# Performance work log

Measured on AMD Instinct MI355X. Metric: run time of the kernel, lower is better.

## Reference

```python
import jax, jax.numpy as jnp
import numpy as np
from jax import lax

NMS_RADIUS = 4
THRESHOLD = 0.005
BORDER = 4
MAX_KP = 1024


def _max_pool(x, r):
    # torch max_pool2d pads with -inf; reduce_window 'SAME' pads with init value.
    w = 2 * r + 1
    return lax.reduce_window(x, -jnp.inf, lax.max, (1, w, w), (1, 1, 1), 'SAME')


def simple_nms(scores, radius):
    zeros = jnp.zeros_like(scores)
    max_mask = scores == _max_pool(scores, radius)
    for _ in range(2):
        supp_mask = _max_pool(max_mask.astype(scores.dtype), radius) > 0
        supp_scores = jnp.where(supp_mask, zeros, scores)
        new_max_mask = supp_scores == _max_pool(supp_scores, radius)
        max_mask = max_mask | (new_max_mask & ~supp_mask)
    return jnp.where(max_mask, scores, zeros)


def sample_descriptors(kp, desc, s):
    """Bilinear grid_sample (align_corners=True, zero padding) + L2 normalize.
    kp: [B,N,2] (x,y) full-resolution pixel coords; desc: [B,C,h,w]."""
    b, c, h, w = desc.shape
    k = kp - s / 2 + 0.5
    gx = k[..., 0] / (w * s - 1) * 2.0 - 1.0
    gy = k[..., 1] / (h * s - 1) * 2.0 - 1.0
    x = (gx + 1.0) * 0.5 * (w - 1)  # align_corners=True mapping
    y = (gy + 1.0) * 0.5 * (h - 1)
    x0 = jnp.floor(x); y0 = jnp.floor(y)
    wx1 = x - x0; wy1 = y - y0
    x0i = x0.astype(jnp.int32); y0i = y0.astype(jnp.int32)

    def tap(d_b, xi, yi):  # d_b [C,h,w]; xi,yi [N] -> [C,N], zero outside
        v = ((xi >= 0) & (xi < w) & (yi >= 0) & (yi < h)).astype(d_b.dtype)
        g = d_b[:, jnp.clip(yi, 0, h - 1), jnp.clip(xi, 0, w - 1)]
        return g * v

    def one(d_b, x0i, y0i, wx1, wy1):
        wx0 = 1.0 - wx1; wy0 = 1.0 - wy1
        return (tap(d_b, x0i, y0i) * (wx0 * wy0)
                + tap(d_b, x0i + 1, y0i) * (wx1 * wy0)
                + tap(d_b, x0i, y0i + 1) * (wx0 * wy1)
                + tap(d_b, x0i + 1, y0i + 1) * (wx1 * wy1))

    out = jax.vmap(one)(desc, x0i, y0i, wx1, wy1)  # [B,C,N]
    n = jnp.maximum(jnp.linalg.norm(out, axis=1, keepdims=True), 1e-12)
    return out / n


def conv1x1(w, b, x):  # Conv1d kernel_size=1: [O,I] @ [B,I,N]
    return jnp.einsum('oi,bin->bon', w, x) + b[None, :, None]


def setup_inputs() -> dict:
    key = jax.random.key(0)
    ks = jax.random.split(key, 13)
    B, H, W = 4, 480, 640
    inp = {
        'scores': jax.random.uniform(ks[0], (B, H, W), jnp.float32),
        'd1': jax.random.normal(ks[1], (B, 64, H // 2, W // 2), jnp.float32),
        'd2': jax.random.normal(ks[2], (B, 128, H // 4, W // 4), jnp.float32),
        'cDa': jax.random.normal(ks[3], (B, 256, H // 8, W // 8), jnp.float32),
        'd4': jax.random.normal(ks[4], (B, 256, H // 16, W // 16), jnp.float32),
        'lin0_w': jax.random.normal(ks[5], (256, 256), jnp.float32) / np.sqrt(256),
        'lin0_b': jax.random.normal(ks[6], (256,), jnp.float32) * 0.01,
        'lin1_w': jax.random.normal(ks[7], (128, 128), jnp.float32) / np.sqrt(128),
        'lin1_b': jax.random.normal(ks[8], (128,), jnp.float32) * 0.01,
        'lin2_w': jax.random.normal(ks[9], (64, 64), jnp.float32) / np.sqrt(64),
        'lin2_b': jax.random.normal(ks[10], (64,), jnp.float32) * 0.01,
        'merge_w': jax.random.normal(ks[11], (256, 704), jnp.float32) / np.sqrt(704),
        'merge_b': jax.random.normal(ks[12], (256,), jnp.float32) * 0.01,
    }
    return inp


def reference(scores, d1, d2, cDa, d4, lin0_w, lin0_b, lin1_w, lin1_b,
              lin2_w, lin2_b, merge_w, merge_b):
    B, H, W = scores.shape
    s = simple_nms(scores, NMS_RADIUS)
    ys, xs = jnp.meshgrid(jnp.arange(H), jnp.arange(W), indexing='ij')
    valid = (ys >= BORDER) & (ys < H - BORDER) & (xs >= BORDER) & (xs < W - BORDER)
    masked = jnp.where(valid[None] & (s > THRESHOLD), s, -1.0)
    top_scores, idx = lax.top_k(masked.reshape(B, -1), MAX_KP)
    kx = (idx % W).astype(jnp.float32)
    ky = (idx // W).astype(jnp.float32)
    kp = jnp.stack([kx, ky], axis=-1)  # [B,K,2] (x,y), i.e. torch.flip(k,[1])
    de1 = sample_descriptors(kp, d1, 2)    # [B,64,K]
    de2 = sample_descriptors(kp, d2, 4)    # [B,128,K]
    de3 = sample_descriptors(kp, cDa, 8)   # [B,256,K]
    de4 = sample_descriptors(kp, d4, 16)   # [B,256,K]
    de4 = conv1x1(lin0_w, lin0_b, de4)
    de2 = conv1x1(lin1_w, lin1_b, de2)
    de1 = conv1x1(lin2_w, lin2_b, de1)
    descriptors = conv1x1(merge_w, merge_b,
                          jnp.concatenate([de1, de2, de3, de4], axis=1))
    return kp, top_scores, descriptors
```

## Files before the change

kernel.cpp:

```cpp
#include <hip/hip_runtime.h>
#include <hip/hip_bf16.h>

#define B 4
#define H 480
#define W 640
#define HW (H*W)
#define BHW (B*H*W)
#define NKP 1024
#define THRESH 0.005f
#define CAP 16384
#define NCOL (B*NKP)
#define KTOT 704

typedef __attribute__((ext_vector_type(8))) short s8v;
typedef __attribute__((ext_vector_type(4))) float f4v;
typedef struct { float x, y; } __attribute__((aligned(4))) f2u;

__device__ __forceinline__ short f2bf(float f) {
    __hip_bfloat16 h = __float2bfloat16(f);
    return *(short*)&h;
}

__device__ __forceinline__ float max3f(float a, float b, float c) {
    return fmaxf(fmaxf(a, b), c);
}
#define MAX9(A, base, str) \
    max3f(max3f((A)[(base)], (A)[(base)+(str)], (A)[(base)+2*(str)]), \
          max3f((A)[(base)+3*(str)], (A)[(base)+4*(str)], (A)[(base)+5*(str)]), \
          max3f((A)[(base)+6*(str)], (A)[(base)+7*(str)], (A)[(base)+8*(str)]))

__global__ void fuse_all(const float* __restrict__ merge_w, const float* __restrict__ merge_b,
                         const float* __restrict__ lin0_w, const float* __restrict__ lin0_b,
                         const float* __restrict__ lin1_w, const float* __restrict__ lin1_b,
                         const float* __restrict__ lin2_w, const float* __restrict__ lin2_b,
                         short* __restrict__ Mw, float* __restrict__ biasf, int* __restrict__ cnt) {
    if (blockIdx.x == 704) {
        int o = threadIdx.x;
        if (o < 4) cnt[o * 64] = 0;
        float acc = merge_b[o];
        for (int k = 0; k < 64; ++k)  acc += merge_w[o * KTOT + k] * lin2_b[k];
        for (int k = 0; k < 128; ++k) acc += merge_w[o * KTOT + 64 + k] * lin1_b[k];
        for (int k = 0; k < 256; ++k) acc += merge_w[o * KTOT + 448 + k] * lin0_b[k];
        biasf[o] = acc;
        return;
    }
    int e = blockIdx.x * 256 + threadIdx.x;
    int o = e / KTOT;
    int j = e - o * KTOT;
    float acc = 0.0f;
    if (j < 64) {
        for (int k = 0; k < 64; ++k) acc += merge_w[o * KTOT + k] * lin2_w[k * 64 + j];
    } else if (j < 192) {
        int jj = j - 64;
        for (int k = 0; k < 128; ++k) acc += merge_w[o * KTOT + 64 + k] * lin1_w[k * 128 + jj];
    } else if (j < 448) {
        acc = merge_w[o * KTOT + j];
    } else {
        int jj = j - 448;
        for (int k = 0; k < 256; ++k) acc += merge_w[o * KTOT + 448 + k] * lin0_w[k * 256 + jj];
    }
    Mw[o * KTOT + j] = f2bf(acc);
}

__global__ __launch_bounds__(256) void nms1(const float* __restrict__ scores,
                                            float* __restrict__ mask) {
    __shared__ float tile[40][40];
    __shared__ float hm[40][32];
    int bz = blockIdx.z;
    int x0 = blockIdx.x * 32, y0 = blockIdx.y * 32;
    const float* sp = scores + bz * HW;
    for (int t = threadIdx.x; t < 1600; t += 256) {
        int ly = t / 40, lx = t - ly * 40;
        int gy = y0 - 4 + ly, gx = x0 - 4 + lx;
        tile[ly][lx] = (gy >= 0 && gy < H && gx >= 0 && gx < W) ? sp[gy * W + gx] : -INFINITY;
    }
    __syncthreads();
    for (int t = threadIdx.x; t < 1280; t += 256) {
        int ly = t >> 5, lx = t & 31;
        hm[ly][lx] = MAX9(&tile[ly][0], lx, 1);
    }
    __syncthreads();
    for (int t = threadIdx.x; t < 1024; t += 256) {
        int ly = t >> 5, lx = t & 31;
        float m = MAX9(&hm[0][0], ly * 32 + lx, 32);
        float s = tile[ly + 4][lx + 4];
        mask[bz * HW + (y0 + ly) * W + x0 + lx] = (s == m) ? 1.0f : 0.0f;
    }
}

__global__ __launch_bounds__(512) void nms2_compact(const float* __restrict__ scores,
                                                    const float* __restrict__ mask0,
                                                    unsigned long long* __restrict__ cand,
                                                    int* __restrict__ cnt) {
    __shared__ float Sm[56 * 56];
    __shared__ float Mm[64 * 64];
    __shared__ float Zm[56 * 56];
    __shared__ float Tm[64 * 56];
    __shared__ int lcnt, gbase;
    int bz = blockIdx.z;
    int x0 = blockIdx.x * 32, y0 = blockIdx.y * 32;
    const float* sp = scores + bz * HW;
    const float* mp = mask0 + bz * HW;
    if (threadIdx.x == 0) lcnt = 0;
    for (int t = threadIdx.x; t < 4096; t += 512) {
        int ly = t >> 6, lx = t & 63;
        int gy = y0 - 16 + ly, gx = x0 - 16 + lx;
        Mm[t] = (gy >= 0 && gy < H && gx >= 0 && gx < W) ? mp[gy * W + gx] : 0.0f;
    }
    for (int t = threadIdx.x; t < 3136; t += 512) {
        int i = t / 56, j = t - i * 56;
        int gy = y0 - 12 + i, gx = x0 - 12 + j;
        Sm[t] = (gy >= 0 && gy < H && gx >= 0 && gx < W) ? sp[gy * W + gx] : -1.0f;
    }
    __syncthreads();
    for (int t = threadIdx.x; t < 3584; t += 512) {
        int i = t / 56, c = t - i * 56;
        Tm[i * 56 + c] = MAX9(Mm, i * 64 + c, 1);
    }
    __syncthreads();
    for (int t = threadIdx.x; t < 3136; t += 512) {
        int i = t / 56, c = t - i * 56;
        float m = MAX9(Tm, i * 56 + c, 56);
        Zm[t] = (m > 0.0f) ? -1.0f : Sm[t];
    }
    __syncthreads();
    for (int t = threadIdx.x; t < 2688; t += 512) {
        int i = t / 48, c = t - i * 48;
        Tm[i * 56 + c] = MAX9(Zm, i * 56 + c, 1);
    }
    __syncthreads();
    for (int t = threadIdx.x; t < 2304; t += 512) {
        int r = t / 48, c = t - r * 48;
        float m = MAX9(Tm, r * 56 + c, 56);
        float Zc = Zm[(r + 4) * 56 + c + 4];
        int mi = (r + 8) * 64 + c + 8;
        bool nm = (Zc == m) && (Zc >= 0.0f);
        Mm[mi] = (Mm[mi] != 0.0f || nm) ? 1.0f : 0.0f;
    }
    __syncthreads();
    for (int t = threadIdx.x; t < 1920; t += 512) {
        int r = t / 40, c = t - r * 40;
        Tm[r * 56 + c] = MAX9(Mm, (r + 8) * 64 + c + 8, 1);
    }
    __syncthreads();
    for (int t = threadIdx.x; t < 1600; t += 512) {
        int r = t / 40, c = t - r * 40;
        float m = MAX9(Tm, r * 56 + c, 56);
        int zi = (r + 8) * 56 + c + 8;
        Zm[zi] = (m > 0.0f) ? -1.0f : Sm[zi];
    }
    __syncthreads();
    for (int t = threadIdx.x; t < 1280; t += 512) {
        int r = t / 32, c = t & 31;
        Tm[r * 56 + c] = MAX9(Zm, (r + 8) * 56 + c + 8, 1);
    }
    __syncthreads();
    unsigned long long keys[2];
    int nl = 0;
    #pragma unroll
    for (int q = 0; q < 2; ++q) {
        int t = threadIdx.x + q * 512;
        int r3 = t >> 5, c = t & 31;
        float m = MAX9(Tm, r3 * 56 + c, 56);
        float Zc = Zm[(r3 + 12) * 56 + c + 12];
        bool fin = (Mm[(r3 + 16) * 64 + c + 16] != 0.0f) || ((Zc == m) && (Zc >= 0.0f));
        int gy = y0 + r3, gx = x0 + c;
        float sc = Sm[(r3 + 12) * 56 + c + 12];
        if (fin && gy >= 4 && gy < H - 4 && gx >= 4 && gx < W - 4 && sc > THRESH) {
            unsigned r = (unsigned)(gy * W + gx);
            unsigned bits = __float_as_uint(sc) | 0x80000000u;
            keys[nl++] = ((unsigned long long)bits << 32) |
                         (unsigned long long)(0xFFFFFFFFu - r);
        }
    }
    int lpos = 0;
    if (nl) lpos = atomicAdd(&lcnt, nl);
    __syncthreads();
    if (threadIdx.x == 0) gbase = (lcnt > 0) ? atomicAdd(&cnt[bz * 64], lcnt) : 0;
    __syncthreads();
    for (int j = 0; j < nl; ++j) {
        int p = gbase + lpos + j;
        if (p < CAP) cand[(size_t)bz * CAP + p] = keys[j];
    }
}

__global__ __launch_bounds__(1024) void topk(const unsigned long long* __restrict__ cand,
                                             const int* __restrict__ cnt,
                                             float* __restrict__ out, int* __restrict__ fidx,
                                             int* __restrict__ perm) {
    __shared__ int hist[2048];
    __shared__ unsigned long long buf[4096];
    __shared__ int scnt, spiv1, spiv2, sabove;
    int b = blockIdx.x, tid = threadIdx.x;
    int m = cnt[b * 64]; if (m > CAP) m = CAP;
    const unsigned long long* cb = cand + (size_t)b * CAP;
    int target = (m < 1024) ? m : 1024;

    hist[tid] = 0; hist[tid + 1024] = 0;
    if (tid == 0) { scnt = 0; spiv1 = 2048; spiv2 = 0; sabove = 0; }
    __syncthreads();
    for (int i = tid; i < m; i += 1024)
        atomicAdd(&hist[(int)(cb[i] >> 53) & 0x7FF], 1);
    __syncthreads();
    for (int d = 1; d < 2048; d <<= 1) {
        int v0 = hist[tid] + ((tid + d < 2048) ? hist[tid + d] : 0);
        int v1 = hist[tid + 1024] + ((tid + 1024 + d < 2048) ? hist[tid + 1024 + d] : 0);
        __syncthreads();
        hist[tid] = v0; hist[tid + 1024] = v1;
        __syncthreads();
    }
    if (target > 0) {
        for (int t = tid; t < 2048; t += 1024) {
            int c = hist[t];
            int cn = (t < 2047) ? hist[t + 1] : 0;
            if (c >= target && cn < target) { spiv1 = t; sabove = cn; }
        }
    }
    __syncthreads();
    int piv1 = spiv1;
    int target2 = target - sabove;
    hist[tid] = 0; hist[tid + 1024] = 0;
    __syncthreads();
    for (int i = tid; i < m; i += 1024) {
        unsigned long long k = cb[i];
        if (((int)(k >> 53) & 0x7FF) == piv1)
            atomicAdd(&hist[(int)(k >> 42) & 0x7FF], 1);
    }
    __syncthreads();
    for (int d = 1; d < 2048; d <<= 1) {
        int v0 = hist[tid] + ((tid + d < 2048) ? hist[tid + d] : 0);
        int v1 = hist[tid + 1024] + ((tid + 1024 + d < 2048) ? hist[tid + 1024 + d] : 0);
        __syncthreads();
        hist[tid] = v0; hist[tid + 1024] = v1;
        __syncthreads();
    }
    if (target > 0) {
        for (int t = tid; t < 2048; t += 1024) {
            int c = hist[t];
            int cn = (t < 2047) ? hist[t + 1] : 0;
            if (c >= target2 && cn < target2) spiv2 = t;
        }
    }
    __syncthreads();
    int piv2 = spiv2;
    for (int i = tid; i < m; i += 1024) {
        unsigned long long k = cb[i];
        int b1 = (int)(k >> 53) & 0x7FF;
        bool sel = (target > 0) &&
                   (b1 > piv1 || (b1 == piv1 && (((int)(k >> 42) & 0x7FF) >= piv2)));
        if (sel) {
            int p = atomicAdd(&scnt, 1);
            if (p < 4096) buf[p] = k;
        }
    }
    __syncthreads();
    int sc_ = scnt; if (sc_ > 4096) sc_ = 4096;
    int ns = 1024; while (ns < sc_) ns <<= 1;
    for (int t = tid; t < ns; t += 1024) if (t >= sc_) buf[t] = 0ULL;
    __syncthreads();
    for (int k = 2; k <= ns; k <<= 1)
        for (int j = k >> 1; j > 0; j >>= 1) {
            __syncthreads();
            for (int t = tid; t < ns; t += 1024) {
                int ixj = t ^ j;
                if (ixj > t) {
                    unsigned long long a = buf[t], bb = buf[ixj];
                    if (((t & k) == 0) ? (a < bb) : (a > bb)) { buf[t] = bb; buf[ixj] = a; }
                }
            }
        }
    __syncthreads();
    unsigned long long key = buf[tid];
    float kx, ky, sc;
    unsigned idx;
    if (key != 0ULL) {
        unsigned ord = (unsigned)(key >> 32);
        sc = __uint_as_float(ord ^ 0x80000000u);
        idx = 0xFFFFFFFFu - (unsigned)(key & 0xFFFFFFFFu);
        kx = (float)(idx % W);
        ky = (float)(idx / W);
    } else {
        sc = -1.0f; idx = 0; kx = 0.0f; ky = 0.0f;
    }
    int bn = b * NKP + tid;
    out[bn * 2 + 0] = kx;
    out[bn * 2 + 1] = ky;
    out[B * NKP * 2 + bn] = sc;
    fidx[bn] = (int)idx;
    __syncthreads();
    unsigned* b32 = (unsigned*)buf;
    b32[tid] = (idx << 10) | (unsigned)tid;
    for (int k = 2; k <= 1024; k <<= 1)
        for (int j = k >> 1; j > 0; j >>= 1) {
            __syncthreads();
            int ixj = tid ^ j;
            if (ixj > tid) {
                unsigned a = b32[tid], bb = b32[ixj];
                if (((tid & k) == 0) ? (a > bb) : (a < bb)) { b32[tid] = bb; b32[ixj] = a; }
            }
        }
    __syncthreads();
    perm[b * NKP + tid] = (int)(b32[tid] & 1023u);
}

__global__ __launch_bounds__(256) void sample_all(const float* __restrict__ d1,
                                                  const float* __restrict__ d2,
                                                  const float* __restrict__ cDa,
                                                  const float* __restrict__ d4,
                                                  const int* __restrict__ fidx,
                                                  const int* __restrict__ perm,
                                                  short* __restrict__ X) {
    int lane = threadIdx.x & 63;
    int wv = threadIdx.x >> 6;
    int seg = blockIdx.y;
    int bid = blockIdx.x;
    int swz = ((bid & 7) << 7) | (bid >> 3);
    int b = swz >> 8;
    int g0 = ((swz & 255) << 2) + wv;

    const float* map; int h, w, s, C, base, nset;
    if (seg == 0)      { map = d1;  h = 240; w = 320; s = 2;  C = 64;  base = 0;   nset = 1; }
    else if (seg == 1) { map = d2;  h = 120; w = 160; s = 4;  C = 128; base = 64;  nset = 2; }
    else if (seg == 2) { map = cDa; h = 60;  w = 80;  s = 8;  C = 256; base = 192; nset = 4; }
    else               { map = d4;  h = 30;  w = 40;  s = 16; C = 256; base = 448; nset = 4; }

    int col = (b << 10) | perm[(b << 10) + g0];
    int idx = fidx[col];
    float kx = (float)(idx % W);
    float ky = (float)(idx / W);
    float kxs = kx - (float)s * 0.5f + 0.5f;
    float kys = ky - (float)s * 0.5f + 0.5f;
    float gx = kxs / (float)(w * s - 1) * 2.0f - 1.0f;
    float gy = kys / (float)(h * s - 1) * 2.0f - 1.0f;
    float x = (gx + 1.0f) * 0.5f * (float)(w - 1);
    float y = (gy + 1.0f) * 0.5f * (float)(h - 1);
    float x0f = floorf(x), y0f = floorf(y);
    int x0 = (int)x0f, y0 = (int)y0f;
    float wx1 = x - x0f, wy1 = y - y0f;
    float wx0 = 1.0f - wx1, wy0 = 1.0f - wy1;
    bool vx0 = (x0 >= 0) && (x0 < w);
    bool vx1 = (x0 + 1 >= 0) && (x0 + 1 < w);
    bool vy0 = (y0 >= 0) && (y0 < h);
    bool vy1 = (y0 + 1 >= 0) && (y0 + 1 < h);
    int xc0 = min(max(x0, 0), w - 1), xc1 = min(max(x0 + 1, 0), w - 1);
    int yc0 = min(max(y0, 0), h - 1), yc1 = min(max(y0 + 1, 0), h - 1);
    float w00 = (vx0 && vy0) ? wx0 * wy0 : 0.0f;
    float w01 = (vx1 && vy0) ? wx1 * wy0 : 0.0f;
    float w10 = (vx0 && vy1) ? wx0 * wy1 : 0.0f;
    float w11 = (vx1 && vy1) ? wx1 * wy1 : 0.0f;
    int xb = min(xc0, w - 2);
    float s0 = (xc0 == xb) ? 1.0f : 0.0f;
    float s1 = (xc1 == xb) ? 1.0f : 0.0f;
    float ax = w00 * s0 + w01 * s1;
    float ay = w00 * (1.0f - s0) + w01 * (1.0f - s1);
    float bx = w10 * s0 + w11 * s1;
    float by = w10 * (1.0f - s0) + w11 * (1.0f - s1);

    size_t hw = (size_t)(h * w);
    const float* pb = map + ((size_t)b * C + lane) * hw;
    size_t off0 = (size_t)yc0 * w + xb;
    size_t off1 = (size_t)yc1 * w + xb;
    size_t cstr = hw << 6;

    f2u q0[4], q1[4];
    #pragma unroll
    for (int j = 0; j < 4; ++j) {
        if (j < nset) {
            const float* p = pb + (size_t)j * cstr;
            q0[j] = *(const f2u*)(p + off0);
            q1[j] = *(const f2u*)(p + off1);
        }
    }
    float vals[4];
    float r = 0.0f;
    #pragma unroll
    for (int j = 0; j < 4; ++j) {
        if (j < nset) {
            vals[j] = q0[j].x * ax + q0[j].y * ay + q1[j].x * bx + q1[j].y * by;
            r += vals[j] * vals[j];
        }
    }
    #pragma unroll
    for (int off = 32; off > 0; off >>= 1) r += __shfl_xor(r, off, 64);
    float denom = fmaxf(sqrtf(r), 1e-12f);
    float inv = 1.0f / denom;
    short* xp = X + (size_t)col * KTOT + base + lane;
    #pragma unroll
    for (int j = 0; j < 4; ++j) {
        if (j < nset) xp[j * 64] = f2bf(vals[j] * inv);
    }
}

__global__ __launch_bounds__(256) void gemm_mfma(const short* __restrict__ Mw,
                                                 const short* __restrict__ X,
                                                 const float* __restrict__ biasf,
                                                 float* __restrict__ out) {
    __shared__ short As[64 * 72];
    __shared__ short Bs[64 * 72];
    int tid = threadIdx.x;
    int lane = tid & 63, w = tid >> 6;
    int r = lane & 15, quad = lane >> 4;
    int rowBase = blockIdx.y * 64, colBase = blockIdx.x * 64;
    int sm = tid >> 2, skq = (tid & 3) << 4;

    const short* pa = Mw + (size_t)(rowBase + sm) * KTOT + skq;
    const short* pb = X + (size_t)(colBase + sm) * KTOT + skq;
    s8v a0 = *(const s8v*)(pa), a1 = *(const s8v*)(pa + 8);
    s8v b0 = *(const s8v*)(pb), b1 = *(const s8v*)(pb + 8);

    f4v acc[4];
    #pragma unroll
    for (int t = 0; t < 4; ++t) acc[t] = (f4v)0.0f;

    for (int kt = 0; kt < 11; ++kt) {
        __syncthreads();
        *(s8v*)&As[sm * 72 + skq + 0] = a0;
        *(s8v*)&As[sm * 72 + skq + 8] = a1;
        *(s8v*)&Bs[sm * 72 + skq + 0] = b0;
        *(s8v*)&Bs[sm * 72 + skq + 8] = b1;
        __syncthreads();
        if (kt < 10) {
            pa += 64; pb += 64;
            a0 = *(const s8v*)(pa); a1 = *(const s8v*)(pa + 8);
            b0 = *(const s8v*)(pb); b1 = *(const s8v*)(pb + 8);
        }
        #pragma unroll
        for (int kk = 0; kk < 2; ++kk) {
            int aoff = (w * 16 + r) * 72 + kk * 32 + quad * 8;
            s8v af = *(const s8v*)&As[aoff];
            #pragma unroll
            for (int t = 0; t < 4; ++t) {
                int boff = (t * 16 + r) * 72 + kk * 32 + quad * 8;
                s8v bf = *(const s8v*)&Bs[boff];
                acc[t] = __builtin_amdgcn_mfma_f32_16x16x32_bf16(af, bf, acc[t], 0, 0, 0);
            }
        }
    }
    #pragma unroll
    for (int t = 0; t < 4; ++t) {
        int colg = colBase + t * 16 + r;
        size_t obase = (size_t)(colg >> 10) * (256 * NKP) + (size_t)(colg & 1023);
        #pragma unroll
        for (int reg = 0; reg < 4; ++reg) {
            int row = rowBase + w * 16 + quad * 4 + reg;
            out[obase + (size_t)row * NKP] = acc[t][reg] + biasf[row];
        }
    }
}

extern "C" void kernel_launch(void* const* d_in, const int* in_sizes, int n_in,
                              void* d_out, int out_size, void* d_ws, size_t ws_size,
                              hipStream_t stream) {
    const float* scores  = (const float*)d_in[0];
    const float* d1      = (const float*)d_in[1];
    const float* d2      = (const float*)d_in[2];
    const float* cDa     = (const float*)d_in[3];
    const float* d4      = (const float*)d_in[4];
    const float* lin0_w  = (const float*)d_in[5];
    const float* lin0_b  = (const float*)d_in[6];
    const float* lin1_w  = (const float*)d_in[7];
    const float* lin1_b  = (const float*)d_in[8];
    const float* lin2_w  = (const float*)d_in[9];
    const float* lin2_b  = (const float*)d_in[10];
    const float* merge_w = (const float*)d_in[11];
    const float* merge_b = (const float*)d_in[12];
    float* out = (float*)d_out;

    char* ws = (char*)d_ws;
    float* MASK = (float*)ws;
    short* Xbuf = (short*)ws;
    unsigned long long* cand  = (unsigned long long*)(ws + 14745600);
    int* cnt                  = (int*)(ws + 15269888);
    int* fidx                 = (int*)(ws + 15401984);
    short* Mw                 = (short*)(ws + 15418368);
    float* biasf              = (float*)(ws + 16139264);
    int* perm                 = (int*)(ws + 16140288);

    dim3 tgrid(W / 32, H / 32, B);

    fuse_all<<<705, 256, 0, stream>>>(merge_w, merge_b, lin0_w, lin0_b, lin1_w, lin1_b,
                                      lin2_w, lin2_b, Mw, biasf, cnt);
    nms1<<<tgrid, 256, 0, stream>>>(scores, MASK);
    nms2_compact<<<tgrid, 512, 0, stream>>>(scores, MASK, cand, cnt);
    topk<<<B, 1024, 0, stream>>>(cand, cnt, out, fidx, perm);
    sample_all<<<dim3(1024, 4), 256, 0, stream>>>(d1, d2, cDa, d4, fidx, perm, Xbuf);
    gemm_mfma<<<dim3(NCOL / 64, 256 / 64), 256, 0, stream>>>(Mw, Xbuf, biasf, out + B * NKP * 3);
}
```

Measured before the change: 353.4 us.

## Transpose d4 to channel-last and replace bitonic sort with bucket counting sort

Adds a kernel that transposes the coarsest descriptor map d4 into pixel-major, channel-contiguous layout, so the seg-3 bilinear taps read 64 contiguous channels per wave instead of strided per-channel planes. Separately, the keypoint ordering in topk swaps a 1024-element shared-memory bitonic sort for a histogram, prefix-scan and scatter bucketed by idx>>10. That removes many barrier rounds. The ordering within a bucket now depends on atomic order, so the result is only approximately sorted by locality. It also adds an extra kernel launch and a write of the transposed map to workspace.

```diff
diff --git a/kernel.cpp b/kernel.cpp
--- a/kernel.cpp
+++ b/kernel.cpp
@@ -60,6 +60,27 @@
         for (int k = 0; k < 256; ++k) acc += merge_w[o * KTOT + 448 + k] * lin0_w[k * 256 + jj];
     }
     Mw[o * KTOT + j] = f2bf(acc);
+}
+
+__global__ __launch_bounds__(256) void transpose_d4(const float* __restrict__ d4,
+                                                    float* __restrict__ d4T) {
+    __shared__ float T[64][65];
+    int b = blockIdx.z;
+    int p0 = blockIdx.x * 64;
+    int c0 = blockIdx.y * 64;
+    for (int t = threadIdx.x; t < 4096; t += 256) {
+        int ch = t >> 6, px = t & 63;
+        int gp = p0 + px;
+        if (gp < 1200)
+            T[ch][px] = d4[((size_t)(b * 256 + c0 + ch)) * 1200 + gp];
+    }
+    __syncthreads();
+    for (int t = threadIdx.x; t < 4096; t += 256) {
+        int px = t >> 6, ch = t & 63;
+        int gp = p0 + px;
+        if (gp < 1200)
+            d4T[((size_t)(b * 1200 + gp)) * 256 + c0 + ch] = T[ch][px];
+    }
 }
 
 __global__ __launch_bounds__(256) void nms1(const float* __restrict__ scores,
@@ -288,25 +309,29 @@
     out[B * NKP * 2 + bn] = sc;
     fidx[bn] = (int)idx;
     __syncthreads();
-    unsigned* b32 = (unsigned*)buf;
-    b32[tid] = (idx << 10) | (unsigned)tid;
-    for (int k = 2; k <= 1024; k <<= 1)
-        for (int j = k >> 1; j > 0; j >>= 1) {
-            __syncthreads();
-            int ixj = tid ^ j;
-            if (ixj > tid) {
-                unsigned a = b32[tid], bb = b32[ixj];
-                if (((tid & k) == 0) ? (a > bb) : (a < bb)) { b32[tid] = bb; b32[ixj] = a; }
-            }
-        }
-    __syncthreads();
-    perm[b * NKP + tid] = (int)(b32[tid] & 1023u);
+    if (tid < 512) { hist[tid] = 0; hist[tid + 1024] = 0; }
+    __syncthreads();
+    int bucket = (int)(idx >> 10);
+    atomicAdd(&hist[bucket], 1);
+    __syncthreads();
+    if (tid < 512) hist[512 + tid] = hist[tid];
+    __syncthreads();
+    for (int d = 1; d < 512; d <<= 1) {
+        int v = 0;
+        if (tid < 512) v = hist[512 + tid] + ((tid >= d) ? hist[512 + tid - d] : 0);
+        __syncthreads();
+        if (tid < 512) hist[512 + tid] = v;
+        __syncthreads();
+    }
+    int intra = atomicAdd(&hist[1024 + bucket], 1);
+    int pos = hist[512 + bucket] - hist[bucket] + intra;
+    perm[b * NKP + pos] = tid;
 }
 
 __global__ __launch_bounds__(256) void sample_all(const float* __restrict__ d1,
                                                   const float* __restrict__ d2,
                                                   const float* __restrict__ cDa,
-                                                  const float* __restrict__ d4,
+                                                  const float* __restrict__ d4T,
                                                   const int* __restrict__ fidx,
                                                   const int* __restrict__ perm,
                                                   short* __restrict__ X) {
@@ -322,7 +347,7 @@
     if (seg == 0)      { map = d1;  h = 240; w = 320; s = 2;  C = 64;  base = 0;   nset = 1; }
     else if (seg == 1) { map = d2;  h = 120; w = 160; s = 4;  C = 128; base = 64;  nset = 2; }
     else if (seg == 2) { map = cDa; h = 60;  w = 80;  s = 8;  C = 256; base = 192; nset = 4; }
-    else               { map = d4;  h = 30;  w = 40;  s = 16; C = 256; base = 448; nset = 4; }
+    else               { map = d4T; h = 30;  w = 40;  s = 16; C = 256; base = 448; nset = 4; }
 
     int col = (b << 10) | perm[(b << 10) + g0];
     int idx = fidx[col];
@@ -348,36 +373,54 @@
     float w01 = (vx1 && vy0) ? wx1 * wy0 : 0.0f;
     float w10 = (vx0 && vy1) ? wx0 * wy1 : 0.0f;
     float w11 = (vx1 && vy1) ? wx1 * wy1 : 0.0f;
-    int xb = min(xc0, w - 2);
-    float s0 = (xc0 == xb) ? 1.0f : 0.0f;
-    float s1 = (xc1 == xb) ? 1.0f : 0.0f;
-    float ax = w00 * s0 + w01 * s1;
-    float ay = w00 * (1.0f - s0) + w01 * (1.0f - s1);
-    float bx = w10 * s0 + w11 * s1;
-    float by = w10 * (1.0f - s0) + w11 * (1.0f - s1);
-
-    size_t hw = (size_t)(h * w);
-    const float* pb = map + ((size_t)b * C + lane) * hw;
-    size_t off0 = (size_t)yc0 * w + xb;
-    size_t off1 = (size_t)yc1 * w + xb;
-    size_t cstr = hw << 6;
-
-    f2u q0[4], q1[4];
-    #pragma unroll
-    for (int j = 0; j < 4; ++j) {
-        if (j < nset) {
-            const float* p = pb + (size_t)j * cstr;
-            q0[j] = *(const f2u*)(p + off0);
-            q1[j] = *(const f2u*)(p + off1);
-        }
-    }
+
     float vals[4];
     float r = 0.0f;
-    #pragma unroll
-    for (int j = 0; j < 4; ++j) {
-        if (j < nset) {
-            vals[j] = q0[j].x * ax + q0[j].y * ay + q1[j].x * bx + q1[j].y * by;
+    if (seg == 3) {
+        const float* pt = d4T + ((size_t)b * 1200) * 256 + lane;
+        size_t o00 = ((size_t)(yc0 * 40 + xc0)) << 8;
+        size_t o01 = ((size_t)(yc0 * 40 + xc1)) << 8;
+        size_t o10 = ((size_t)(yc1 * 40 + xc0)) << 8;
+        size_t o11 = ((size_t)(yc1 * 40 + xc1)) << 8;
+        float q00[4], q01[4], q10[4], q11[4];
+        #pragma unroll
+        for (int j = 0; j < 4; ++j) {
+            q00[j] = pt[o00 + j * 64]; q01[j] = pt[o01 + j * 64];
+            q10[j] = pt[o10 + j * 64]; q11[j] = pt[o11 + j * 64];
+        }
+        #pragma unroll
+        for (int j = 0; j < 4; ++j) {
+            vals[j] = q00[j] * w00 + q01[j] * w01 + q10[j] * w10 + q11[j] * w11;
             r += vals[j] * vals[j];
+        }
+    } else {
+        int xb = min(xc0, w - 2);
+        float s0 = (xc0 == xb) ? 1.0f : 0.0f;
+        float s1 = (xc1 == xb) ? 1.0f : 0.0f;
+        float ax = w00 * s0 + w01 * s1;
+        float ay = w00 * (1.0f - s0) + w01 * (1.0f - s1);
+        float bx = w10 * s0 + w11 * s1;
+        float by = w10 * (1.0f - s0) + w11 * (1.0f - s1);
+        size_t hw = (size_t)(h * w);
+        const float* pb = map + ((size_t)b * C + lane) * hw;
+        size_t off0 = (size_t)yc0 * w + xb;
+        size_t off1 = (size_t)yc1 * w + xb;
+        size_t cstr = hw << 6;
+        f2u q0[4], q1[4];
+        #pragma unroll
+        for (int j = 0; j < 4; ++j) {
+            if (j < nset) {
+                const float* p = pb + (size_t)j * cstr;
+                q0[j] = *(const f2u*)(p + off0);
+                q1[j] = *(const f2u*)(p + off1);
+            }
+        }
+        #pragma unroll
+        for (int j = 0; j < 4; ++j) {
+            if (j < nset) {
+                vals[j] = q0[j].x * ax + q0[j].y * ay + q1[j].x * bx + q1[j].y * by;
+                r += vals[j] * vals[j];
+            }
         }
     }
     #pragma unroll
@@ -469,6 +512,7 @@
     char* ws = (char*)d_ws;
     float* MASK = (float*)ws;
     short* Xbuf = (short*)ws;
+    float* d4T  = (float*)(ws + 6291456);
     unsigned long long* cand  = (unsigned long long*)(ws + 14745600);
     int* cnt                  = (int*)(ws + 15269888);
     int* fidx                 = (int*)(ws + 15401984);
@@ -480,9 +524,10 @@
 
     fuse_all<<<705, 256, 0, stream>>>(merge_w, merge_b, lin0_w, lin0_b, lin1_w, lin1_b,
                                       lin2_w, lin2_b, Mw, biasf, cnt);
+    transpose_d4<<<dim3(19, 4, 4), 256, 0, stream>>>(d4, d4T);
     nms1<<<tgrid, 256, 0, stream>>>(scores, MASK);
     nms2_compact<<<tgrid, 512, 0, stream>>>(scores, MASK, cand, cnt);
     topk<<<B, 1024, 0, stream>>>(cand, cnt, out, fidx, perm);
-    sample_all<<<dim3(1024, 4), 256, 0, stream>>>(d1, d2, cDa, d4, fidx, perm, Xbuf);
+    sample_all<<<dim3(1024, 4), 256, 0, stream>>>(d1, d2, cDa, d4T, fidx, perm, Xbuf);
     gemm_mfma<<<dim3(NCOL / 64, 256 / 64), 256, 0, stream>>>(Mw, Xbuf, biasf, out + B * NKP * 3);
 }
```

Result: no change. 352.9 us (-0.2%).
